# Kernel optimization log

Measured on AMD Instinct MI355X. Metric: run time of the kernel, lower is better.

The kernel has to match this reference:

```python
import jax, jax.numpy as jnp
import numpy as np

EPS = 1e-6
RES_CONN = True


def _layernorm(x, g, b):
    mu = jnp.mean(x, axis=-1, keepdims=True)
    var = jnp.var(x, axis=-1, keepdims=True)
    return (x - mu) * jax.lax.rsqrt(var + EPS) * g + b


def setup_inputs() -> dict:
    key = jax.random.key(0)
    ks = jax.random.split(key, 8)
    L, H, V, B, T = 2, 1024, 32000, 4, 512
    s = 0.02
    return {
        "x": jax.random.randint(ks[0], (B, T), 0, V, dtype=jnp.int32),
        "emb": jax.random.normal(ks[1], (V, H), jnp.float32) * s,
        "ln_g": jnp.ones((L, H), jnp.float32),
        "ln_b": jnp.zeros((L, H), jnp.float32),
        "Wl": jax.random.normal(ks[2], (L, 2 * H, 4 * H), jnp.float32) * s,
        "bl": jnp.zeros((L, 4 * H), jnp.float32),
        "Wo": jax.random.normal(ks[3], (L, H, H), jnp.float32) * s,
        "bo": jnp.zeros((L, H), jnp.float32),
        "W1": jax.random.normal(ks[4], (L, H, 4 * H), jnp.float32) * s,
        "b1": jnp.zeros((L, 4 * H), jnp.float32),
        "W2": jax.random.normal(ks[5], (L, 4 * H, H), jnp.float32) * s,
        "b2": jnp.zeros((L, H), jnp.float32),
    }


def reference(x, emb, ln_g, ln_b, Wl, bl, Wo, bo, W1, b1, W2, b2):
    # x: [B, T] int token ids. Returns dec_logits [B, T, V].
    B, T = x.shape
    L, H = ln_g.shape
    x_emb = emb[x]                      # [B, T, H] (dropout inactive: eval mode)
    xs = jnp.swapaxes(x_emb, 0, 1)      # [T, B, H]

    def step(carry, xt):
        c_prev, h_prev = carry          # each [L, B, H]
        cs, hs = [], []
        prev_input = jnp.zeros_like(xt)
        inp = xt                        # [B, H]
        for m in range(L):
            xn = _layernorm(inp, ln_g[m], ln_b[m])
            z = jnp.concatenate([xn, h_prev[m]], axis=-1) @ Wl[m] + bl[m]
            z = z.reshape(B, 4, H)
            i_g = jax.nn.sigmoid(z[:, 0])
            f_g = jax.nn.sigmoid(z[:, 1])
            o_g = jax.nn.sigmoid(z[:, 2])
            c = f_g * c_prev[m] + i_g * jnp.tanh(z[:, 3])
            h = o_g * jnp.tanh(c)
            ff = jax.nn.relu(xn @ W1[m] + b1[m]) @ W2[m] + b2[m]
            y = inp + ff + h @ Wo[m] + bo[m]
            if RES_CONN:
                y = y + prev_input
            prev_input = inp
            inp = y
            cs.append(c)
            hs.append(h)
        logits = inp @ emb.T            # tied embedding: [B, V]
        return (jnp.stack(cs), jnp.stack(hs)), logits

    carry0 = (jnp.zeros((L, B, H), x_emb.dtype), jnp.zeros((L, B, H), x_emb.dtype))
    _, logits = jax.lax.scan(step, carry0, xs)   # logits [T, B, V]
    return jnp.swapaxes(logits, 0, 1)            # [B, T, V]
```

## Files before the change

kernel.cpp:

```cpp
#include <hip/hip_runtime.h>

typedef unsigned short u16;
typedef short bf16x8 __attribute__((ext_vector_type(8)));
typedef unsigned short ushort8 __attribute__((ext_vector_type(8)));
typedef unsigned short us4 __attribute__((ext_vector_type(4)));
typedef unsigned u32x4 __attribute__((ext_vector_type(4)));
typedef float fx4 __attribute__((ext_vector_type(4)));

#define DEVI __device__ __forceinline__

enum { BB = 4, TT = 512, HH = 1024, VV = 32000, H4 = 4096 };
enum { WSTR = 1032 };

DEVI u16 f2bf(float f) {
    union { float f; unsigned u; } x; x.f = f;
    unsigned r = x.u + 0x7fff + ((x.u >> 16) & 1);
    return (u16)(r >> 16);
}
DEVI float bf2f(u16 u) {
    union { unsigned u; float f; } x; x.u = ((unsigned)u) << 16;
    return x.f;
}
DEVI float sigm(float x) { return 1.f / (1.f + __expf(-x)); }

DEVI unsigned ald_u32(const unsigned* p) { return __hip_atomic_load(p, __ATOMIC_RELAXED, __HIP_MEMORY_SCOPE_AGENT); }
DEVI void ast_u32(unsigned* p, unsigned v) { __hip_atomic_store(p, v, __ATOMIC_RELAXED, __HIP_MEMORY_SCOPE_AGENT); }

DEVI void ld4cc(const unsigned* p, u32x4* out) {
    asm volatile("global_load_dwordx4 %0, %1, off sc0 sc1" : "=v"(*out) : "v"(p));
}

DEVI void poll4096(const unsigned* base, unsigned want, u16* st, int tid) {
    const unsigned* p0 = base + tid * 8;
    const unsigned* p1 = p0 + 4;
    u32x4 v0, v1;
    ld4cc(p0, &v0); ld4cc(p1, &v1);
    asm volatile("s_waitcnt vmcnt(0)" ::: "memory");
    __builtin_amdgcn_sched_barrier(0);
    for (;;) {
        bool o0 = ((v0[0]>>16)==want)&((v0[1]>>16)==want)&((v0[2]>>16)==want)&((v0[3]>>16)==want);
        bool o1 = ((v1[0]>>16)==want)&((v1[1]>>16)==want)&((v1[2]>>16)==want)&((v1[3]>>16)==want);
        if (o0 & o1) break;
        __builtin_amdgcn_s_sleep(1);
        if (!o0) ld4cc(p0, &v0);
        if (!o1) ld4cc(p1, &v1);
        asm volatile("s_waitcnt vmcnt(0)" ::: "memory");
        __builtin_amdgcn_sched_barrier(0);
    }
    int wi = tid * 8;
    u16* d = st + (wi >> 10) * WSTR + (wi & 1023);
    *(us4*)d       = (us4){(u16)v0[0], (u16)v0[1], (u16)v0[2], (u16)v0[3]};
    *(us4*)(d + 4) = (us4){(u16)v1[0], (u16)v1[1], (u16)v1[2], (u16)v1[3]};
}

DEVI unsigned poll_word(const unsigned* p, unsigned want) {
    unsigned v = ald_u32(p);
    while ((v >> 16) != want) { __builtin_amdgcn_s_sleep(1); v = ald_u32(p); }
    return v & 0xFFFFu;
}

DEVI void gates64(const u16* wl, const u16* st, float* fb, int tid) {
    int lane = tid & 63, wv = tid >> 6;
    int rt = wv & 3, kh = wv >> 2;
    fx4 acc = {0.f, 0.f, 0.f, 0.f};
    int aoff = (rt * 16 + (lane & 15)) * WSTR + (lane >> 4) * 8;
    int boff = (lane & 3) * WSTR + (lane >> 4) * 8;
#pragma unroll
    for (int kt = 0; kt < 16; kt++) {
        int k0 = (kh * 16 + kt) * 32;
        bf16x8 a = *(const bf16x8*)(wl + aoff + k0);
        bf16x8 b = *(const bf16x8*)(st + boff + k0);
        acc = __builtin_amdgcn_mfma_f32_16x16x32_bf16(a, b, acc, 0, 0, 0);
    }
    int col = lane & 15;
    if (col < 4) {
        int r0 = rt * 16 + (lane >> 4) * 4;
#pragma unroll
        for (int ri = 0; ri < 4; ri++) fb[kh * 256 + (r0 + ri) * 4 + col] = acc[ri];
    }
}

__global__ void transpose_cast(const float* __restrict__ src, u16* __restrict__ dst, int R, int C) {
    __shared__ float tile[32][33];
    int c0 = blockIdx.x * 32, r0 = blockIdx.y * 32;
    int x = threadIdx.x, y = threadIdx.y;
#pragma unroll
    for (int i = 0; i < 32; i += 8) tile[y + i][x] = src[(size_t)(r0 + y + i) * C + c0 + x];
    __syncthreads();
#pragma unroll
    for (int i = 0; i < 32; i += 8) dst[(size_t)(c0 + y + i) * R + r0 + x] = f2bf(tile[x][y + i]);
}

__global__ void cast_bf16(const float* __restrict__ src, u16* __restrict__ dst, int n) {
    int i = blockIdx.x * 256 + threadIdx.x;
    if (i < n) dst[i] = f2bf(src[i]);
}

__global__ void zero_buf(float* p, int n) {
    int i = blockIdx.x * 256 + threadIdx.x;
    if (i < n) p[i] = 0.f;
}

__global__ __launch_bounds__(256) void gather_ln(const int* __restrict__ x, const float* __restrict__ emb,
                                                 const float* __restrict__ g, const float* __restrict__ b,
                                                 float* __restrict__ xe, u16* __restrict__ xn0) {
    int t = blockIdx.x, bb = blockIdx.y;
    int row = x[bb * TT + t];
    const float* e = emb + (size_t)row * HH;
    float v[4]; float s = 0.f, s2 = 0.f;
#pragma unroll
    for (int p = 0; p < 4; p++) { v[p] = e[p * 256 + threadIdx.x]; s += v[p]; s2 += v[p] * v[p]; }
    __shared__ float ls[4], ls2[4];
    for (int off = 32; off; off >>= 1) { s += __shfl_xor(s, off); s2 += __shfl_xor(s2, off); }
    int w = threadIdx.x >> 6, lane = threadIdx.x & 63;
    if (lane == 0) { ls[w] = s; ls2[w] = s2; }
    __syncthreads();
    s = ls[0] + ls[1] + ls[2] + ls[3];
    s2 = ls2[0] + ls2[1] + ls2[2] + ls2[3];
    float mu = s * (1.f / HH);
    float var = s2 * (1.f / HH) - mu * mu;
    float rs = rsqrtf(var + 1e-6f);
    size_t base = ((size_t)t * BB + bb) * HH;
#pragma unroll
    for (int p = 0; p < 4; p++) {
        int j = p * 256 + threadIdx.x;
        xe[base + j] = v[p];
        xn0[base + j] = f2bf((v[p] - mu) * rs * g[j] + b[j]);
    }
}

template <int MODE>
__global__ __launch_bounds__(256) void gemm_bt(const u16* __restrict__ A, const u16* __restrict__ Bt,
                                               float* __restrict__ Cf, u16* __restrict__ Cb,
                                               const float* __restrict__ bias, int M, int N, int K) {
    __shared__ u16 ldsA[128 * 40];
    __shared__ u16 ldsB[128 * 40];
    const int tid = threadIdx.x;
    const int m0 = blockIdx.y * 128, n0 = blockIdx.x * 128;
    const int lane = tid & 63, wid = tid >> 6;
    const int wr = wid >> 1, wc = wid & 1;
    const int l15 = lane & 15, lk = (lane >> 4) * 8;
    fx4 acc[4][4];
#pragma unroll
    for (int a = 0; a < 4; a++)
#pragma unroll
        for (int b = 0; b < 4; b++) { fx4 z = {0.f, 0.f, 0.f, 0.f}; acc[a][b] = z; }

    const int arow = tid >> 2, acol = (tid & 3) * 8;
    for (int k0 = 0; k0 < K; k0 += 32) {
#pragma unroll
        for (int p = 0; p < 2; p++) {
            int r = arow + p * 64;
            ushort8 va = *(const ushort8*)(A + (size_t)(m0 + r) * K + k0 + acol);
            *(ushort8*)&ldsA[r * 40 + acol] = va;
            ushort8 vb = *(const ushort8*)(Bt + (size_t)(n0 + r) * K + k0 + acol);
            *(ushort8*)&ldsB[r * 40 + acol] = vb;
        }
        __syncthreads();
        bf16x8 af[4], bfr[4];
#pragma unroll
        for (int mi = 0; mi < 4; mi++) af[mi] = *(const bf16x8*)&ldsA[(wr * 64 + mi * 16 + l15) * 40 + lk];
#pragma unroll
        for (int ni = 0; ni < 4; ni++) bfr[ni] = *(const bf16x8*)&ldsB[(wc * 64 + ni * 16 + l15) * 40 + lk];
#pragma unroll
        for (int mi = 0; mi < 4; mi++)
#pragma unroll
            for (int ni = 0; ni < 4; ni++)
                acc[mi][ni] = __builtin_amdgcn_mfma_f32_16x16x32_bf16(af[mi], bfr[ni], acc[mi][ni], 0, 0, 0);
        __syncthreads();
    }
#pragma unroll
    for (int mi = 0; mi < 4; mi++) {
#pragma unroll
        for (int ni = 0; ni < 4; ni++) {
#pragma unroll
            for (int r = 0; r < 4; r++) {
                int gr = m0 + wr * 64 + mi * 16 + (lane >> 4) * 4 + r;
                int gc = n0 + wc * 64 + ni * 16 + l15;
                float v = acc[mi][ni][r];
                if (MODE == 0) {
                    Cf[(size_t)gr * N + gc] = v + bias[gc];
                } else if (MODE == 1) {
                    float u = v + bias[gc];
                    Cb[(size_t)gr * N + gc] = f2bf(u > 0.f ? u : 0.f);
                } else if (MODE == 2) {
                    Cf[(size_t)gr * N + gc] += v;
                } else {
                    int b = gr & 3, t = gr >> 2;
                    Cf[((size_t)b * TT + t) * VV + gc] = v;
                }
            }
        }
    }
}

__global__ __launch_bounds__(512, 1) void lstm_pipe(
    const u16* __restrict__ Wh0T, const u16* __restrict__ Wo0T,
    const u16* __restrict__ Wx1T, const u16* __restrict__ Wh1T,
    const float* __restrict__ pz_all, const float* __restrict__ xe, const float* __restrict__ ff0,
    const float* __restrict__ lng, const float* __restrict__ lnb,
    const float* __restrict__ bl, const float* __restrict__ bo,
    float* __restrict__ y0_all, u16* __restrict__ xn1, u16* __restrict__ H1bf,
    unsigned* __restrict__ R) {
    __shared__ u16 wlds[64 * WSTR];
    __shared__ u16 stg[4 * WSTR];
    __shared__ float fb[1536];

    const int bid = blockIdx.x;
    const int tid = threadIdx.x;
    const int lane = tid & 63, wv = tid >> 6;

    unsigned* RH0 = R;
    unsigned* RH1 = R + 16384;
    unsigned* RPART = R + 32768;
    unsigned* RXN = R + 36864;
    unsigned* RZX = R + 102400;
    unsigned* PROGZX = R + 364544;
    unsigned* PROGL1 = R + 366592;

    if (bid < 64) {
        const int w = bid;
        {
            int row = tid >> 3, kc = tid & 7;
            int gr = (row >> 4) * 1024 + w * 16 + (row & 15);
            const uint4* s = (const uint4*)(Wh0T + (size_t)gr * 1024 + kc * 128);
            uint4* d = (uint4*)(wlds + row * WSTR + kc * 128);
#pragma unroll
            for (int i = 0; i < 16; i++) d[i] = s[i];
        }
        uint4 woA[2], woB[2];
#pragma unroll
        for (int jj = 0; jj < 2; jj++) {
            const u16* src = Wo0T + (size_t)(w * 16 + wv * 2 + jj) * 1024 + lane * 16;
            woA[jj] = *(const uint4*)src;
            woB[jj] = *(const uint4*)(src + 8);
        }
        float lgR = 0.f, lbR = 0.f, boR = 0.f;
        if (tid < 64) {
            int x = tid >> 2;
            lgR = lng[1024 + w * 16 + x];
            lbR = lnb[1024 + w * 16 + x];
            boR = bo[w * 16 + x];
            fb[1104 + tid] = 0.f;
        }
        __syncthreads();

        for (int s = 0; s < TT + 2; s++) {
            const bool doG = (s < TT);
            const bool doY = (s >= 1 && s <= TT);
            const bool doX = (s >= 2);
            if (doX && (s & 7) == 0 && tid < 64) {
                for (;;) {
                    unsigned p = ald_u32(PROGZX + tid * 32);
#pragma unroll
                    for (int off = 1; off < 64; off <<= 1) {
                        unsigned o = (unsigned)__shfl_xor((int)p, off);
                        p = p < o ? p : o;
                    }
                    if ((int)p >= s - 9) break;
                    __builtin_amdgcn_s_sleep(8);
                }
            }
            float pzv[4] = {0.f,0.f,0.f,0.f}, xev = 0.f, ffv = 0.f;
            if (tid < 64) {
                int x = tid >> 2, b = tid & 3;
                if (doG) {
#pragma unroll
                    for (int g = 0; g < 4; g++)
                        pzv[g] = pz_all[((size_t)s * 4 + b) * 4096 + g * 1024 + w * 16 + x];
                }
                if (doY) {
                    size_t base = ((size_t)(s - 1) * 4 + b) * 1024 + w * 16 + x;
                    xev = xe[base]; ffv = ff0[base];
                }
            }
            if (s <= TT) poll4096(RH0 + ((s + 3) & 3) * 4096, (unsigned)s, stg, tid);
            if (doX) {
                const unsigned* p = RPART + ((s - 2) & 3) * 1024 + tid * 2;
                unsigned hi = poll_word(p, (unsigned)(s - 1));
                unsigned lo = poll_word(p + 1, (unsigned)(s - 1));
                union { unsigned u; float f; } c; c.u = (hi << 16) | lo;
                fb[576 + tid] = c.f;
            }
            __syncthreads();
            if (doX && tid < 8) {
                int b = tid & 3, kind = tid >> 2;
                float S = 0.f;
                for (int i = 0; i < 64; i++) S += fb[576 + i * 8 + b * 2 + kind];
                fb[1096 + kind * 4 + b] = S;
            }
            if (doG) gates64(wlds, stg, fb, tid);
            if (doY) {
                float yacc[2][4] = {};
                ushort8 h8[4][2];
#pragma unroll
                for (int b = 0; b < 4; b++) {
                    h8[b][0] = *(const ushort8*)(stg + b * WSTR + lane * 16);
                    h8[b][1] = *(const ushort8*)(stg + b * WSTR + lane * 16 + 8);
                }
#pragma unroll
                for (int jj = 0; jj < 2; jj++) {
                    const ushort8 wA = *(const ushort8*)&woA[jj];
                    const ushort8 wB = *(const ushort8*)&woB[jj];
#pragma unroll
                    for (int m = 0; m < 8; m++) {
                        float wf = bf2f(wA[m]), wg = bf2f(wB[m]);
#pragma unroll
                        for (int b = 0; b < 4; b++)
                            yacc[jj][b] += wf * bf2f(h8[b][0][m]) + wg * bf2f(h8[b][1][m]);
                    }
                }
#pragma unroll
                for (int jj = 0; jj < 2; jj++)
#pragma unroll
                    for (int b = 0; b < 4; b++) {
                        float v = yacc[jj][b];
#pragma unroll
                        for (int off = 1; off < 64; off <<= 1) v += __shfl_xor(v, off);
                        if (lane == 0) fb[512 + (wv * 2 + jj) * 4 + b] = v;
                    }
            }
            __syncthreads();
            if (tid < 64) {
                int x = tid >> 2, b = tid & 3;
                if (doG) {
                    float z0 = fb[(0*16+x)*4+b] + fb[256+(0*16+x)*4+b] + pzv[0];
                    float z1 = fb[(1*16+x)*4+b] + fb[256+(1*16+x)*4+b] + pzv[1];
                    float z2 = fb[(2*16+x)*4+b] + fb[256+(2*16+x)*4+b] + pzv[2];
                    float z3 = fb[(3*16+x)*4+b] + fb[256+(3*16+x)*4+b] + pzv[3];
                    float ig = sigm(z0), fg = sigm(z1), og = sigm(z2), gg = tanhf(z3);
                    float c = fg * fb[1104 + tid] + ig * gg;
                    fb[1104 + tid] = c;
                    float h = og * tanhf(c);
                    ast_u32(&RH0[(s & 3) * 4096 + b * 1024 + w * 16 + x],
                            ((unsigned)(s + 1) << 16) | f2bf(h));
                }
                if (doY) {
                    float y = fb[512 + x * 4 + b] + xev + ffv + boR;
                    y0_all[((size_t)(s - 1) * 4 + b) * 1024 + w * 16 + x] = y;
                    fb[1168 + ((s - 1) & 1) * 64 + x * 4 + b] = y;
                    float sv = y, sq = y * y;
#pragma unroll
                    for (int off = 4; off < 64; off <<= 1) { sv += __shfl_xor(sv, off); sq += __shfl_xor(sq, off); }
                    if (tid < 4) {
                        unsigned tg = (unsigned)s << 16;
                        unsigned* pb = RPART + ((s - 1) & 3) * 1024 + w * 16 + tid * 4;
                        union { float f; unsigned u; } c1, c2; c1.f = sv; c2.f = sq;
                        ast_u32(pb + 0, tg | (c1.u >> 16));
                        ast_u32(pb + 1, tg | (c1.u & 0xFFFFu));
                        ast_u32(pb + 2, tg | (c2.u >> 16));
                        ast_u32(pb + 3, tg | (c2.u & 0xFFFFu));
                    }
                }
                if (doX) {
                    int u = s - 2;
                    float Ssum = fb[1096 + b], Ssq = fb[1100 + b];
                    float mu = Ssum * (1.f / 1024.f);
                    float rs = rsqrtf(Ssq * (1.f / 1024.f) - mu * mu + 1e-6f);
                    float yv = fb[1168 + (u & 1) * 64 + x * 4 + b];
                    float xnv = (yv - mu) * rs * lgR + lbR;
                    u16 xb = f2bf(xnv);
                    xn1[(size_t)u * 4096 + b * 1024 + w * 16 + x] = xb;
                    ast_u32(&RXN[(u & 15) * 4096 + b * 1024 + w * 16 + x],
                            ((unsigned)(u + 1) << 16) | xb);
                }
            }
            __syncthreads();
        }
    } else if (bid < 128) {
        const int wz = bid - 64;
        {
            int row = tid >> 3, kc = tid & 7;
            int gr = (row >> 4) * 1024 + wz * 16 + (row & 15);
            const uint4* s = (const uint4*)(Wx1T + (size_t)gr * 1024 + kc * 128);
            uint4* d = (uint4*)(wlds + row * WSTR + kc * 128);
#pragma unroll
            for (int i = 0; i < 16; i++) d[i] = s[i];
        }
        if (tid < 64) fb[1300 + tid] = bl[4096 + (tid >> 4) * 1024 + wz * 16 + (tid & 15)];
        __syncthreads();

        for (int t = 0; t < TT; t++) {
            if ((t & 7) == 0 && tid == 0) {
                while ((int)ald_u32(PROGL1) < t - 6) __builtin_amdgcn_s_sleep(8);
            }
            poll4096(RXN + (t & 15) * 4096, (unsigned)(t + 1), stg, tid);
            __syncthreads();
            gates64(wlds, stg, fb, tid);
            __syncthreads();
            if (tid < 256) {
                int lr = tid >> 2, b = tid & 3;
                float v = fb[lr * 4 + b] + fb[256 + lr * 4 + b] + fb[1300 + lr];
                ast_u32(&RZX[(t & 15) * 16384 + wz * 256 + tid],
                        ((unsigned)(t + 1) << 16) | f2bf(v));
            }
            if (tid == 0) ast_u32(PROGZX + wz * 32, (unsigned)(t + 1));
            __syncthreads();
        }
    } else {
        const int w1 = bid - 128;
        {
            int row = tid >> 3, kc = tid & 7;
            int gr = (row >> 4) * 1024 + w1 * 16 + (row & 15);
            const uint4* s = (const uint4*)(Wh1T + (size_t)gr * 1024 + kc * 128);
            uint4* d = (uint4*)(wlds + row * WSTR + kc * 128);
#pragma unroll
            for (int i = 0; i < 16; i++) d[i] = s[i];
        }
        if (tid < 64) fb[576 + tid] = 0.f;
        __syncthreads();

        for (int v = 0; v < TT; v++) {
            poll4096(RH1 + ((v + 3) & 3) * 4096, (unsigned)v, stg, tid);
            if (tid < 256) {
                const unsigned* p = RZX + (v & 15) * 16384 + w1 * 256 + tid;
                fb[1024 + (v & 1) * 256 + tid] = bf2f((u16)poll_word(p, (unsigned)(v + 1)));
            }
            __syncthreads();
            gates64(wlds, stg, fb, tid);
            __syncthreads();
            if (tid < 64) {
                int x = tid >> 2, b = tid & 3;
                int zb = 1024 + (v & 1) * 256;
                float z0 = fb[(0*16+x)*4+b] + fb[256+(0*16+x)*4+b] + fb[zb + (0*16+x)*4+b];
                float z1 = fb[(1*16+x)*4+b] + fb[256+(1*16+x)*4+b] + fb[zb + (1*16+x)*4+b];
                float z2 = fb[(2*16+x)*4+b] + fb[256+(2*16+x)*4+b] + fb[zb + (2*16+x)*4+b];
                float z3 = fb[(3*16+x)*4+b] + fb[256+(3*16+x)*4+b] + fb[zb + (3*16+x)*4+b];
                float ig = sigm(z0), fg = sigm(z1), og = sigm(z2), gg = tanhf(z3);
                float c = fg * fb[576 + tid] + ig * gg;
                fb[576 + tid] = c;
                float h = og * tanhf(c);
                u16 hb = f2bf(h);
                H1bf[(size_t)v * 4096 + b * 1024 + w1 * 16 + x] = hb;
                ast_u32(&RH1[(v & 3) * 4096 + b * 1024 + w1 * 16 + x],
                        ((unsigned)(v + 1) << 16) | hb);
            }
            if (bid == 128 && tid == 0) ast_u32(PROGL1, (unsigned)(v + 1));
            __syncthreads();
        }
    }
}

__global__ void p1_add(float* __restrict__ y, const float* __restrict__ xe,
                       const float* __restrict__ b2_1, const float* __restrict__ bo_1) {
    int idx = blockIdx.x * 256 + threadIdx.x;
    int j = idx & (HH - 1);
    y[idx] += xe[idx] + b2_1[j] + bo_1[j];
}

__global__ void p2_cast(const float* __restrict__ y, u16* __restrict__ o) {
    int idx = blockIdx.x * 256 + threadIdx.x;
    o[idx] = f2bf(y[idx]);
}

extern "C" void kernel_launch(void* const* d_in, const int* in_sizes, int n_in,
                              void* d_out, int out_size, void* d_ws, size_t ws_size,
                              hipStream_t stream) {
    const int* x = (const int*)d_in[0];
    const float* emb = (const float*)d_in[1];
    const float* ln_g = (const float*)d_in[2];
    const float* ln_b = (const float*)d_in[3];
    const float* Wl = (const float*)d_in[4];
    const float* bl = (const float*)d_in[5];
    const float* Wo = (const float*)d_in[6];
    const float* bo = (const float*)d_in[7];
    const float* W1 = (const float*)d_in[8];
    const float* b1 = (const float*)d_in[9];
    const float* W2 = (const float*)d_in[10];
    const float* b2 = (const float*)d_in[11];
    float* out = (float*)d_out;

    char* wp = (char*)d_ws;
    auto alloc = [&](size_t bytes) { void* p = wp; wp += (bytes + 255) & ~(size_t)255; return p; };
    const size_t MBT = (size_t)TT * BB;
    float* xe     = (float*)alloc(MBT * HH * 4);
    float* pre_z0 = (float*)alloc(MBT * H4 * 4);
    float* ff0    = (float*)alloc(MBT * HH * 4);
    float* y0_all = (float*)alloc(MBT * HH * 4);
    u16* xn0      = (u16*)alloc(MBT * HH * 2);
    u16* xn1      = (u16*)alloc(MBT * HH * 2);
    u16* U0       = (u16*)alloc(MBT * H4 * 2);
    u16* U1       = (u16*)alloc(MBT * H4 * 2);
    u16* H1bf     = (u16*)alloc(MBT * HH * 2);
    u16* Y1bf     = (u16*)alloc(MBT * HH * 2);
    unsigned* R   = (unsigned*)alloc(366624 * 4);
    u16* WlxT0 = (u16*)alloc((size_t)H4 * HH * 2);
    u16* WlhT0 = (u16*)alloc((size_t)H4 * HH * 2);
    u16* WlxT1 = (u16*)alloc((size_t)H4 * HH * 2);
    u16* WlhT1 = (u16*)alloc((size_t)H4 * HH * 2);
    u16* Wo0T  = (u16*)alloc((size_t)HH * HH * 2);
    u16* Wo1T  = (u16*)alloc((size_t)HH * HH * 2);
    u16* W10T  = (u16*)alloc((size_t)H4 * HH * 2);
    u16* W11T  = (u16*)alloc((size_t)H4 * HH * 2);
    u16* W20T  = (u16*)alloc((size_t)HH * H4 * 2);
    u16* W21T  = (u16*)alloc((size_t)HH * H4 * 2);
    u16* embB  = (u16*)alloc((size_t)VV * HH * 2);

    dim3 tb(32, 8);
    transpose_cast<<<dim3(128, 32), tb, 0, stream>>>(Wl, WlxT0, HH, H4);
    transpose_cast<<<dim3(128, 32), tb, 0, stream>>>(Wl + 1024 * 4096, WlhT0, HH, H4);
    transpose_cast<<<dim3(128, 32), tb, 0, stream>>>(Wl + 2048 * 4096, WlxT1, HH, H4);
    transpose_cast<<<dim3(128, 32), tb, 0, stream>>>(Wl + 3072 * 4096, WlhT1, HH, H4);
    transpose_cast<<<dim3(32, 32), tb, 0, stream>>>(Wo, Wo0T, HH, HH);
    transpose_cast<<<dim3(32, 32), tb, 0, stream>>>(Wo + 1024 * 1024, Wo1T, HH, HH);
    transpose_cast<<<dim3(128, 32), tb, 0, stream>>>(W1, W10T, HH, H4);
    transpose_cast<<<dim3(128, 32), tb, 0, stream>>>(W1 + 1024 * 4096, W11T, HH, H4);
    transpose_cast<<<dim3(32, 128), tb, 0, stream>>>(W2, W20T, H4, HH);
    transpose_cast<<<dim3(32, 128), tb, 0, stream>>>(W2 + 4096 * 1024, W21T, H4, HH);
    cast_bf16<<<(VV * HH + 255) / 256, 256, 0, stream>>>(emb, embB, VV * HH);
    gather_ln<<<dim3(TT, BB), 256, 0, stream>>>(x, emb, ln_g, ln_b, xe, xn0);

    gemm_bt<0><<<dim3(32, 16), 256, 0, stream>>>(xn0, WlxT0, pre_z0, nullptr, bl, 2048, 4096, 1024);
    gemm_bt<1><<<dim3(32, 16), 256, 0, stream>>>(xn0, W10T, nullptr, U0, b1, 2048, 4096, 1024);
    gemm_bt<0><<<dim3(8, 16), 256, 0, stream>>>(U0, W20T, ff0, nullptr, b2, 2048, 1024, 4096);

    zero_buf<<<1433, 256, 0, stream>>>((float*)R, 366624);

    lstm_pipe<<<192, 512, 0, stream>>>(WlhT0, Wo0T, WlxT1, WlhT1, pre_z0, xe, ff0,
                                       ln_g, ln_b, bl, bo, y0_all, xn1, H1bf, R);

    gemm_bt<1><<<dim3(32, 16), 256, 0, stream>>>(xn1, W11T, nullptr, U1, b1 + 4096, 2048, 4096, 1024);
    p1_add<<<8192, 256, 0, stream>>>(y0_all, xe, b2 + 1024, bo + 1024);
    gemm_bt<2><<<dim3(8, 16), 256, 0, stream>>>(U1, W21T, y0_all, nullptr, nullptr, 2048, 1024, 4096);
    gemm_bt<2><<<dim3(8, 16), 256, 0, stream>>>(H1bf, Wo1T, y0_all, nullptr, nullptr, 2048, 1024, 1024);
    p2_cast<<<8192, 256, 0, stream>>>(y0_all, Y1bf);
    gemm_bt<3><<<dim3(250, 16), 256, 0, stream>>>(Y1bf, embB, out, nullptr, nullptr, 2048, 32000, 1024);
}
```

Baseline: 4.032 ms.

## Split layer-0 recurrence from Wo/LayerNorm work into dedicated block group

Layer-0 LSTM blocks now run only the recurrent gate computation. The h@Wo projection, residual sum and layer-1 LayerNorm move to a new group of 64 blocks, so the grid grows from 192 to 256 persistent blocks. The h ring deepens to 8 slots and a new PROGY progress counter provides backpressure. Progress signals are published earlier, gate buffers are double-buffered to drop a barrier, and poll sleep intervals are lengthened. The aim is to shorten the serial critical path of the layer-0 recurrence, at the cost of more blocks, more cross-block flag traffic and extra poll latency.

```diff
diff --git a/kernel.cpp b/kernel.cpp
--- a/kernel.cpp
+++ b/kernel.cpp
@@ -41,7 +41,7 @@
         bool o0 = ((v0[0]>>16)==want)&((v0[1]>>16)==want)&((v0[2]>>16)==want)&((v0[3]>>16)==want);
         bool o1 = ((v1[0]>>16)==want)&((v1[1]>>16)==want)&((v1[2]>>16)==want)&((v1[3]>>16)==want);
         if (o0 & o1) break;
-        __builtin_amdgcn_s_sleep(1);
+        __builtin_amdgcn_s_sleep(4);
         if (!o0) ld4cc(p0, &v0);
         if (!o1) ld4cc(p1, &v1);
         asm volatile("s_waitcnt vmcnt(0)" ::: "memory");
@@ -55,7 +55,7 @@
 
 DEVI unsigned poll_word(const unsigned* p, unsigned want) {
     unsigned v = ald_u32(p);
-    while ((v >> 16) != want) { __builtin_amdgcn_s_sleep(1); v = ald_u32(p); }
+    while ((v >> 16) != want) { __builtin_amdgcn_s_sleep(2); v = ald_u32(p); }
     return v & 0xFFFFu;
 }
 
@@ -204,19 +204,19 @@
     unsigned* __restrict__ R) {
     __shared__ u16 wlds[64 * WSTR];
     __shared__ u16 stg[4 * WSTR];
-    __shared__ float fb[1536];
+    __shared__ float fb[1664];
 
     const int bid = blockIdx.x;
     const int tid = threadIdx.x;
-    const int lane = tid & 63, wv = tid >> 6;
 
     unsigned* RH0 = R;
-    unsigned* RH1 = R + 16384;
-    unsigned* RPART = R + 32768;
-    unsigned* RXN = R + 36864;
-    unsigned* RZX = R + 102400;
-    unsigned* PROGZX = R + 364544;
-    unsigned* PROGL1 = R + 366592;
+    unsigned* RH1 = R + 32768;
+    unsigned* RPART = R + 49152;
+    unsigned* RXN = R + 53248;
+    unsigned* RZX = R + 118784;
+    unsigned* PROGY = R + 380928;
+    unsigned* PROGZX = R + 382976;
+    unsigned* PROGL1 = R + 385024;
 
     if (bid < 64) {
         const int w = bid;
@@ -228,147 +228,152 @@
 #pragma unroll
             for (int i = 0; i < 16; i++) d[i] = s[i];
         }
-        uint4 woA[2], woB[2];
-#pragma unroll
-        for (int jj = 0; jj < 2; jj++) {
-            const u16* src = Wo0T + (size_t)(w * 16 + wv * 2 + jj) * 1024 + lane * 16;
-            woA[jj] = *(const uint4*)src;
-            woB[jj] = *(const uint4*)(src + 8);
-        }
-        float lgR = 0.f, lbR = 0.f, boR = 0.f;
-        if (tid < 64) {
-            int x = tid >> 2;
-            lgR = lng[1024 + w * 16 + x];
-            lbR = lnb[1024 + w * 16 + x];
-            boR = bo[w * 16 + x];
-            fb[1104 + tid] = 0.f;
-        }
+        if (tid < 64) fb[1024 + tid] = 0.f;
         __syncthreads();
 
-        for (int s = 0; s < TT + 2; s++) {
-            const bool doG = (s < TT);
-            const bool doY = (s >= 1 && s <= TT);
-            const bool doX = (s >= 2);
-            if (doX && (s & 7) == 0 && tid < 64) {
+        for (int s = 0; s < TT; s++) {
+            if ((s & 3) == 0 && tid < 64) {
                 for (;;) {
-                    unsigned p = ald_u32(PROGZX + tid * 32);
+                    unsigned p = ald_u32(PROGY + tid * 32);
 #pragma unroll
                     for (int off = 1; off < 64; off <<= 1) {
                         unsigned o = (unsigned)__shfl_xor((int)p, off);
                         p = p < o ? p : o;
                     }
-                    if ((int)p >= s - 9) break;
+                    if ((int)p >= s - 4) break;
                     __builtin_amdgcn_s_sleep(8);
                 }
             }
-            float pzv[4] = {0.f,0.f,0.f,0.f}, xev = 0.f, ffv = 0.f;
+            float pzv[4] = {0.f, 0.f, 0.f, 0.f};
             if (tid < 64) {
                 int x = tid >> 2, b = tid & 3;
-                if (doG) {
-#pragma unroll
-                    for (int g = 0; g < 4; g++)
-                        pzv[g] = pz_all[((size_t)s * 4 + b) * 4096 + g * 1024 + w * 16 + x];
+#pragma unroll
+                for (int g = 0; g < 4; g++)
+                    pzv[g] = pz_all[((size_t)s * 4 + b) * 4096 + g * 1024 + w * 16 + x];
+            }
+            poll4096(RH0 + ((s + 7) & 7) * 4096, (unsigned)s, stg, tid);
+            __syncthreads();
+            float* gbuf = fb + (s & 1) * 512;
+            gates64(wlds, stg, gbuf, tid);
+            __syncthreads();
+            if (tid < 64) {
+                int x = tid >> 2, b = tid & 3;
+                float z0 = gbuf[(0*16+x)*4+b] + gbuf[256+(0*16+x)*4+b] + pzv[0];
+                float z1 = gbuf[(1*16+x)*4+b] + gbuf[256+(1*16+x)*4+b] + pzv[1];
+                float z2 = gbuf[(2*16+x)*4+b] + gbuf[256+(2*16+x)*4+b] + pzv[2];
+                float z3 = gbuf[(3*16+x)*4+b] + gbuf[256+(3*16+x)*4+b] + pzv[3];
+                float ig = sigm(z0), fg = sigm(z1), og = sigm(z2), gg = tanhf(z3);
+                float c = fg * fb[1024 + tid] + ig * gg;
+                fb[1024 + tid] = c;
+                float h = og * tanhf(c);
+                ast_u32(&RH0[(s & 7) * 4096 + b * 1024 + w * 16 + x],
+                        ((unsigned)(s + 1) << 16) | f2bf(h));
+            }
+        }
+    } else if (bid < 128) {
+        const int wy = bid - 64;
+        {
+            int row = tid >> 5, kc = tid & 31;
+            const uint4* s = (const uint4*)(Wo0T + (size_t)(wy * 16 + row) * 1024 + kc * 32);
+            uint4* d = (uint4*)(wlds + row * WSTR + kc * 32);
+            d[0] = s[0]; d[1] = s[1]; d[2] = s[2]; d[3] = s[3];
+        }
+        float lgR = 0.f, lbR = 0.f, boR = 0.f;
+        if (tid < 64) {
+            int x = tid >> 2;
+            lgR = lng[1024 + wy * 16 + x];
+            lbR = lnb[1024 + wy * 16 + x];
+            boR = bo[wy * 16 + x];
+        }
+        __syncthreads();
+
+        for (int t = 0; t <= TT; t++) {
+            const bool doDot = (t < TT);
+            const bool doLN = (t >= 1);
+            if ((t & 7) == 0 && tid < 64) {
+                for (;;) {
+                    unsigned p = ald_u32(PROGZX + tid * 32);
+#pragma unroll
+                    for (int off = 1; off < 64; off <<= 1) {
+                        unsigned o = (unsigned)__shfl_xor((int)p, off);
+                        p = p < o ? p : o;
+                    }
+                    if ((int)p >= t - 8) break;
+                    __builtin_amdgcn_s_sleep(8);
                 }
-                if (doY) {
-                    size_t base = ((size_t)(s - 1) * 4 + b) * 1024 + w * 16 + x;
-                    xev = xe[base]; ffv = ff0[base];
+            }
+            float xev = 0.f, ffv = 0.f;
+            if (doDot && tid < 64) {
+                int x = tid >> 2, b = tid & 3;
+                size_t base = ((size_t)t * 4 + b) * 1024 + wy * 16 + x;
+                xev = xe[base]; ffv = ff0[base];
+            }
+            if (doDot) poll4096(RH0 + (t & 7) * 4096, (unsigned)(t + 1), stg, tid);
+            __syncthreads();
+            if (doDot && tid == 0) ast_u32(PROGY + wy * 32, (unsigned)(t + 1));
+            if (doDot) {
+                int out = tid >> 3, c = tid & 7;
+                const u16* wrow = wlds + (out >> 2) * WSTR + c * 128;
+                const u16* hrow = stg + (out & 3) * WSTR + c * 128;
+                float acc = 0.f;
+#pragma unroll
+                for (int m = 0; m < 16; m++) {
+                    ushort8 w8 = *(const ushort8*)(wrow + m * 8);
+                    ushort8 h8 = *(const ushort8*)(hrow + m * 8);
+#pragma unroll
+                    for (int q = 0; q < 8; q++) acc += bf2f(w8[q]) * bf2f(h8[q]);
                 }
-            }
-            if (s <= TT) poll4096(RH0 + ((s + 3) & 3) * 4096, (unsigned)s, stg, tid);
-            if (doX) {
-                const unsigned* p = RPART + ((s - 2) & 3) * 1024 + tid * 2;
-                unsigned hi = poll_word(p, (unsigned)(s - 1));
-                unsigned lo = poll_word(p + 1, (unsigned)(s - 1));
-                union { unsigned u; float f; } c; c.u = (hi << 16) | lo;
-                fb[576 + tid] = c.f;
-            }
-            __syncthreads();
-            if (doX && tid < 8) {
+                acc += __shfl_xor(acc, 1); acc += __shfl_xor(acc, 2); acc += __shfl_xor(acc, 4);
+                if (c == 0) fb[512 + out] = acc;
+            }
+            if (doLN) {
+                const unsigned* p = RPART + ((t - 1) & 3) * 1024 + tid * 2;
+                unsigned hi = poll_word(p, (unsigned)t);
+                unsigned lo = poll_word(p + 1, (unsigned)t);
+                union { unsigned u; float f; } cv; cv.u = (hi << 16) | lo;
+                fb[tid] = cv.f;
+            }
+            __syncthreads();
+            if (doLN && tid < 8) {
                 int b = tid & 3, kind = tid >> 2;
                 float S = 0.f;
-                for (int i = 0; i < 64; i++) S += fb[576 + i * 8 + b * 2 + kind];
-                fb[1096 + kind * 4 + b] = S;
-            }
-            if (doG) gates64(wlds, stg, fb, tid);
-            if (doY) {
-                float yacc[2][4] = {};
-                ushort8 h8[4][2];
-#pragma unroll
-                for (int b = 0; b < 4; b++) {
-                    h8[b][0] = *(const ushort8*)(stg + b * WSTR + lane * 16);
-                    h8[b][1] = *(const ushort8*)(stg + b * WSTR + lane * 16 + 8);
+                for (int i = 0; i < 64; i++) S += fb[i * 8 + b * 2 + kind];
+                fb[704 + kind * 4 + b] = S;
+            }
+            if (doDot && tid < 64) {
+                int x = tid >> 2, b = tid & 3;
+                float y = fb[512 + tid] + xev + ffv + boR;
+                y0_all[((size_t)t * 4 + b) * 1024 + wy * 16 + x] = y;
+                fb[576 + (t & 1) * 64 + tid] = y;
+                float sv = y, sq = y * y;
+#pragma unroll
+                for (int off = 4; off < 64; off <<= 1) { sv += __shfl_xor(sv, off); sq += __shfl_xor(sq, off); }
+                if (tid < 4) {
+                    unsigned tg = (unsigned)(t + 1) << 16;
+                    unsigned* pb = RPART + (t & 3) * 1024 + wy * 16 + tid * 4;
+                    union { float f; unsigned u; } c1, c2; c1.f = sv; c2.f = sq;
+                    ast_u32(pb + 0, tg | (c1.u >> 16));
+                    ast_u32(pb + 1, tg | (c1.u & 0xFFFFu));
+                    ast_u32(pb + 2, tg | (c2.u >> 16));
+                    ast_u32(pb + 3, tg | (c2.u & 0xFFFFu));
                 }
-#pragma unroll
-                for (int jj = 0; jj < 2; jj++) {
-                    const ushort8 wA = *(const ushort8*)&woA[jj];
-                    const ushort8 wB = *(const ushort8*)&woB[jj];
-#pragma unroll
-                    for (int m = 0; m < 8; m++) {
-                        float wf = bf2f(wA[m]), wg = bf2f(wB[m]);
-#pragma unroll
-                        for (int b = 0; b < 4; b++)
-                            yacc[jj][b] += wf * bf2f(h8[b][0][m]) + wg * bf2f(h8[b][1][m]);
-                    }
-                }
-#pragma unroll
-                for (int jj = 0; jj < 2; jj++)
-#pragma unroll
-                    for (int b = 0; b < 4; b++) {
-                        float v = yacc[jj][b];
-#pragma unroll
-                        for (int off = 1; off < 64; off <<= 1) v += __shfl_xor(v, off);
-                        if (lane == 0) fb[512 + (wv * 2 + jj) * 4 + b] = v;
-                    }
-            }
-            __syncthreads();
-            if (tid < 64) {
+            }
+            __syncthreads();
+            if (doLN && tid < 64) {
                 int x = tid >> 2, b = tid & 3;
-                if (doG) {
-                    float z0 = fb[(0*16+x)*4+b] + fb[256+(0*16+x)*4+b] + pzv[0];
-                    float z1 = fb[(1*16+x)*4+b] + fb[256+(1*16+x)*4+b] + pzv[1];
-                    float z2 = fb[(2*16+x)*4+b] + fb[256+(2*16+x)*4+b] + pzv[2];
-                    float z3 = fb[(3*16+x)*4+b] + fb[256+(3*16+x)*4+b] + pzv[3];
-                    float ig = sigm(z0), fg = sigm(z1), og = sigm(z2), gg = tanhf(z3);
-                    float c = fg * fb[1104 + tid] + ig * gg;
-                    fb[1104 + tid] = c;
-                    float h = og * tanhf(c);
-                    ast_u32(&RH0[(s & 3) * 4096 + b * 1024 + w * 16 + x],
-                            ((unsigned)(s + 1) << 16) | f2bf(h));
-                }
-                if (doY) {
-                    float y = fb[512 + x * 4 + b] + xev + ffv + boR;
-                    y0_all[((size_t)(s - 1) * 4 + b) * 1024 + w * 16 + x] = y;
-                    fb[1168 + ((s - 1) & 1) * 64 + x * 4 + b] = y;
-                    float sv = y, sq = y * y;
-#pragma unroll
-                    for (int off = 4; off < 64; off <<= 1) { sv += __shfl_xor(sv, off); sq += __shfl_xor(sq, off); }
-                    if (tid < 4) {
-                        unsigned tg = (unsigned)s << 16;
-                        unsigned* pb = RPART + ((s - 1) & 3) * 1024 + w * 16 + tid * 4;
-                        union { float f; unsigned u; } c1, c2; c1.f = sv; c2.f = sq;
-                        ast_u32(pb + 0, tg | (c1.u >> 16));
-                        ast_u32(pb + 1, tg | (c1.u & 0xFFFFu));
-                        ast_u32(pb + 2, tg | (c2.u >> 16));
-                        ast_u32(pb + 3, tg | (c2.u & 0xFFFFu));
-                    }
-                }
-                if (doX) {
-                    int u = s - 2;
-                    float Ssum = fb[1096 + b], Ssq = fb[1100 + b];
-                    float mu = Ssum * (1.f / 1024.f);
-                    float rs = rsqrtf(Ssq * (1.f / 1024.f) - mu * mu + 1e-6f);
-                    float yv = fb[1168 + (u & 1) * 64 + x * 4 + b];
-                    float xnv = (yv - mu) * rs * lgR + lbR;
-                    u16 xb = f2bf(xnv);
-                    xn1[(size_t)u * 4096 + b * 1024 + w * 16 + x] = xb;
-                    ast_u32(&RXN[(u & 15) * 4096 + b * 1024 + w * 16 + x],
-                            ((unsigned)(u + 1) << 16) | xb);
-                }
-            }
-            __syncthreads();
-        }
-    } else if (bid < 128) {
-        const int wz = bid - 64;
+                int u = t - 1;
+                float mu = fb[704 + b] * (1.f / 1024.f);
+                float rs = rsqrtf(fb[708 + b] * (1.f / 1024.f) - mu * mu + 1e-6f);
+                float yv = fb[576 + (u & 1) * 64 + tid];
+                float xnv = (yv - mu) * rs * lgR + lbR;
+                u16 xb = f2bf(xnv);
+                xn1[(size_t)u * 4096 + b * 1024 + wy * 16 + x] = xb;
+                ast_u32(&RXN[(u & 15) * 4096 + b * 1024 + wy * 16 + x],
+                        ((unsigned)(u + 1) << 16) | xb);
+            }
+        }
+    } else if (bid < 192) {
+        const int wz = bid - 128;
         {
             int row = tid >> 3, kc = tid & 7;
             int gr = (row >> 4) * 1024 + wz * 16 + (row & 15);
@@ -377,7 +382,7 @@
 #pragma unroll
             for (int i = 0; i < 16; i++) d[i] = s[i];
         }
-        if (tid < 64) fb[1300 + tid] = bl[4096 + (tid >> 4) * 1024 + wz * 16 + (tid & 15)];
+        if (tid < 64) fb[1536 + tid] = bl[4096 + (tid >> 4) * 1024 + wz * 16 + (tid & 15)];
         __syncthreads();
 
         for (int t = 0; t < TT; t++) {
@@ -388,17 +393,17 @@
             __syncthreads();
             gates64(wlds, stg, fb, tid);
             __syncthreads();
+            if (tid == 0) ast_u32(PROGZX + wz * 32, (unsigned)(t + 1));
             if (tid < 256) {
                 int lr = tid >> 2, b = tid & 3;
-                float v = fb[lr * 4 + b] + fb[256 + lr * 4 + b] + fb[1300 + lr];
+                float v = fb[lr * 4 + b] + fb[256 + lr * 4 + b] + fb[1536 + lr];
                 ast_u32(&RZX[(t & 15) * 16384 + wz * 256 + tid],
                         ((unsigned)(t + 1) << 16) | f2bf(v));
             }
-            if (tid == 0) ast_u32(PROGZX + wz * 32, (unsigned)(t + 1));
             __syncthreads();
         }
     } else {
-        const int w1 = bid - 128;
+        const int w1 = bid - 192;
         {
             int row = tid >> 3, kc = tid & 7;
             int gr = (row >> 4) * 1024 + w1 * 16 + (row & 15);
@@ -407,7 +412,7 @@
 #pragma unroll
             for (int i = 0; i < 16; i++) d[i] = s[i];
         }
-        if (tid < 64) fb[576 + tid] = 0.f;
+        if (tid < 64) fb[1600 + tid] = 0.f;
         __syncthreads();
 
         for (int v = 0; v < TT; v++) {
@@ -417,26 +422,26 @@
                 fb[1024 + (v & 1) * 256 + tid] = bf2f((u16)poll_word(p, (unsigned)(v + 1)));
             }
             __syncthreads();
-            gates64(wlds, stg, fb, tid);
+            if (bid == 192 && tid == 0) ast_u32(PROGL1, (unsigned)(v + 1));
+            float* gbuf = fb + (v & 1) * 512;
+            gates64(wlds, stg, gbuf, tid);
             __syncthreads();
             if (tid < 64) {
                 int x = tid >> 2, b = tid & 3;
-                int zb = 1024 + (v & 1) * 256;
-                float z0 = fb[(0*16+x)*4+b] + fb[256+(0*16+x)*4+b] + fb[zb + (0*16+x)*4+b];
-                float z1 = fb[(1*16+x)*4+b] + fb[256+(1*16+x)*4+b] + fb[zb + (1*16+x)*4+b];
-                float z2 = fb[(2*16+x)*4+b] + fb[256+(2*16+x)*4+b] + fb[zb + (2*16+x)*4+b];
-                float z3 = fb[(3*16+x)*4+b] + fb[256+(3*16+x)*4+b] + fb[zb + (3*16+x)*4+b];
+                const float* zb = fb + 1024 + (v & 1) * 256;
+                float z0 = gbuf[(0*16+x)*4+b] + gbuf[256+(0*16+x)*4+b] + zb[(0*16+x)*4+b];
+                float z1 = gbuf[(1*16+x)*4+b] + gbuf[256+(1*16+x)*4+b] + zb[(1*16+x)*4+b];
+                float z2 = gbuf[(2*16+x)*4+b] + gbuf[256+(2*16+x)*4+b] + zb[(2*16+x)*4+b];
+                float z3 = gbuf[(3*16+x)*4+b] + gbuf[256+(3*16+x)*4+b] + zb[(3*16+x)*4+b];
                 float ig = sigm(z0), fg = sigm(z1), og = sigm(z2), gg = tanhf(z3);
-                float c = fg * fb[576 + tid] + ig * gg;
-                fb[576 + tid] = c;
+                float c = fg * fb[1600 + tid] + ig * gg;
+                fb[1600 + tid] = c;
                 float h = og * tanhf(c);
                 u16 hb = f2bf(h);
                 H1bf[(size_t)v * 4096 + b * 1024 + w1 * 16 + x] = hb;
                 ast_u32(&RH1[(v & 3) * 4096 + b * 1024 + w1 * 16 + x],
                         ((unsigned)(v + 1) << 16) | hb);
             }
-            if (bid == 128 && tid == 0) ast_u32(PROGL1, (unsigned)(v + 1));
-            __syncthreads();
         }
     }
 }
@@ -483,7 +488,7 @@
     u16* U1       = (u16*)alloc(MBT * H4 * 2);
     u16* H1bf     = (u16*)alloc(MBT * HH * 2);
     u16* Y1bf     = (u16*)alloc(MBT * HH * 2);
-    unsigned* R   = (unsigned*)alloc(366624 * 4);
+    unsigned* R   = (unsigned*)alloc(385056 * 4);
     u16* WlxT0 = (u16*)alloc((size_t)H4 * HH * 2);
     u16* WlhT0 = (u16*)alloc((size_t)H4 * HH * 2);
     u16* WlxT1 = (u16*)alloc((size_t)H4 * HH * 2);
@@ -514,9 +519,9 @@
     gemm_bt<1><<<dim3(32, 16), 256, 0, stream>>>(xn0, W10T, nullptr, U0, b1, 2048, 4096, 1024);
     gemm_bt<0><<<dim3(8, 16), 256, 0, stream>>>(U0, W20T, ff0, nullptr, b2, 2048, 1024, 4096);
 
-    zero_buf<<<1433, 256, 0, stream>>>((float*)R, 366624);
-
-    lstm_pipe<<<192, 512, 0, stream>>>(WlhT0, Wo0T, WlxT1, WlhT1, pre_z0, xe, ff0,
+    zero_buf<<<1505, 256, 0, stream>>>((float*)R, 385056);
+
+    lstm_pipe<<<256, 512, 0, stream>>>(WlhT0, Wo0T, WlxT1, WlhT1, pre_z0, xe, ff0,
                                        ln_g, ln_b, bl, bo, y0_all, xn1, H1bf, R);
 
     gemm_bt<1><<<dim3(32, 16), 256, 0, stream>>>(xn1, W11T, nullptr, U1, b1 + 4096, 2048, 4096, 1024);
```

Measured after the change: 3.693 ms. 1.09x faster.
